# Kernel tuning notes

Hardware: AMD Instinct MI355X
Metric: run time of the kernel (lower is better)

## Reference

```python
import jax, jax.numpy as jnp
import numpy as np

B, S, H, P2 = 64, 512, 768, 46  # batch, seq, hidden, num_p*2


def setup_inputs() -> dict:
    key = jax.random.key(0)
    k1, k2, k3, k4 = jax.random.split(key, 4)
    hidden_states = jax.random.normal(k1, (B, S, H), dtype=jnp.float32)
    # subject start/end indices must lie within the valid (masked-in) prefix
    lengths = jax.random.randint(k2, (B,), S // 4, S + 1)  # cue lengths per sample
    input_mask = (jnp.arange(S)[None, :] < lengths[:, None]).astype(jnp.int32)
    ids = jax.random.randint(k3, (B, 2), 0, S // 4)
    batch_subject_ids = jnp.sort(ids, axis=1).astype(jnp.int32)
    W = jax.random.normal(k4, (P2, H), dtype=jnp.float32) * (1.0 / np.sqrt(H))
    b = jnp.zeros((P2,), dtype=jnp.float32)
    return {"hidden_states": hidden_states, "batch_subject_ids": batch_subject_ids,
            "input_mask": input_mask, "W": W, "b": b}


def reference(hidden_states, batch_subject_ids, input_mask, W, b):
    # per-sample subject embedding: h[b, start] + h[b, end]  -> [B, H]
    batch_idx = jnp.arange(hidden_states.shape[0])
    s = (hidden_states[batch_idx, batch_subject_ids[:, 0]]
         + hidden_states[batch_idx, batch_subject_ids[:, 1]])
    # broadcast-add s to the first cue_len positions of each sample
    cue_len = jnp.sum(input_mask, axis=1)  # [B]
    pos_mask = (jnp.arange(hidden_states.shape[1])[None, :] < cue_len[:, None])  # [B, S]
    h = hidden_states + s[:, None, :] * pos_mask[:, :, None].astype(hidden_states.dtype)
    # linear + sigmoid^4 (dropout is identity in eval mode)
    logits = jnp.einsum('bsh,ph->bsp', h, W) + b
    return jax.nn.sigmoid(logits) ** 4
```

## Files before the change

kernel.cpp:

```cpp
#include <hip/hip_runtime.h>

#define SEQ 512
#define HID 768
#define P2  46
#define BLK 256
#define WST 776

typedef short bf16x8 __attribute__((ext_vector_type(8)));
typedef float f32x4  __attribute__((ext_vector_type(4)));

__device__ __forceinline__ unsigned short f2bf(float f) {
  union { float f; unsigned int u; } v; v.f = f;
  return (unsigned short)((v.u + 0x7FFFu + ((v.u >> 16) & 1u)) >> 16);
}

__global__ __launch_bounds__(BLK) void fused_kernel(const float* __restrict__ h,
                                                    const int* __restrict__ ids,
                                                    const int* __restrict__ mask,
                                                    const float* __restrict__ W,
                                                    const float* __restrict__ bias,
                                                    float* __restrict__ out) {
  __shared__ __align__(16) unsigned short wlds[48 * WST];
  __shared__ __align__(16) float s_lds[HID];
  __shared__ float q_lds[48];

  const int tid  = threadIdx.x;
  const int lane = tid & 63, wv = tid >> 6;
  const int mr   = lane & 15, qd = lane >> 4;
  const int row0 = blockIdx.x * 64;
  const int b    = row0 >> 9;
  const int rowa = row0 + (wv << 4) + mr;
  const float* hrow = h + (size_t)rowa * HID + (qd << 3);

  for (int i = tid; i < WST; i += BLK)
    ((unsigned int*)(wlds + 46 * WST))[i] = 0u;
  for (int i = tid; i < (P2 * HID) / 4; i += BLK) {
    int f = i * 4;
    int r = f / HID;
    int c = f - r * HID;
    float4 w4 = *(const float4*)(W + (size_t)r * HID + c);
    ushort4 v;
    v.x = f2bf(w4.x); v.y = f2bf(w4.y); v.z = f2bf(w4.z); v.w = f2bf(w4.w);
    *(ushort4*)&wlds[r * WST + c] = v;
  }
  {
    int i0 = ids[b * 2 + 0], i1 = ids[b * 2 + 1];
    const float* r0 = h + ((size_t)b * SEQ + i0) * HID;
    const float* r1 = h + ((size_t)b * SEQ + i1) * HID;
    #pragma unroll
    for (int j = 0; j < HID / BLK; ++j) {
      int k = tid + j * BLK;
      s_lds[k] = r0[k] + r1[k];
    }
  }
  __syncthreads();

  if (tid < P2 * 4) {
    int p = tid >> 2, kq = tid & 3;
    const float4* wp = (const float4*)(W + (size_t)p * HID + kq * 192);
    float acc = 0.f;
    #pragma unroll 8
    for (int j = 0; j < 48; ++j) {
      float4 w4 = wp[j];
      int k = kq * 192 + j * 4;
      acc += s_lds[k] * w4.x + s_lds[k + 1] * w4.y
           + s_lds[k + 2] * w4.z + s_lds[k + 3] * w4.w;
    }
    acc += __shfl_xor(acc, 1, 64);
    acc += __shfl_xor(acc, 2, 64);
    if (kq == 0) q_lds[p] = acc;
  }
  __syncthreads();

  f32x4 acc[3];
  #pragma unroll
  for (int nt = 0; nt < 3; ++nt) acc[nt] = f32x4{0.f, 0.f, 0.f, 0.f};

  #pragma unroll
  for (int half = 0; half < 2; ++half) {
    const float* hb = hrow + half * 384;
    float4 abuf[24];
    #pragma unroll
    for (int i = 0; i < 24; ++i)
      abuf[i] = *(const float4*)(hb + (i >> 1) * 32 + (i & 1) * 4);
    #pragma unroll
    for (int it = 0; it < 12; ++it) {
      bf16x8 a;
      {
        float4 x0 = abuf[2 * it], x1 = abuf[2 * it + 1];
        a[0] = (short)f2bf(x0.x); a[1] = (short)f2bf(x0.y);
        a[2] = (short)f2bf(x0.z); a[3] = (short)f2bf(x0.w);
        a[4] = (short)f2bf(x1.x); a[5] = (short)f2bf(x1.y);
        a[6] = (short)f2bf(x1.z); a[7] = (short)f2bf(x1.w);
      }
      #pragma unroll
      for (int nt = 0; nt < 3; ++nt) {
        bf16x8 bb = *(const bf16x8*)&wlds[((nt << 4) + mr) * WST
                                          + half * 384 + it * 32 + (qd << 3)];
        acc[nt] = __builtin_amdgcn_mfma_f32_16x16x32_bf16(a, bb, acc[nt], 0, 0, 0);
      }
    }
  }

  int mrow[4];
  #pragma unroll
  for (int i = 0; i < 4; ++i)
    mrow[i] = mask[row0 + (wv << 4) + (qd << 2) + i];

  #pragma unroll
  for (int nt = 0; nt < 3; ++nt) {
    int p = (nt << 4) + mr;
    if (p < P2) {
      float bv = bias[p];
      float qv = q_lds[p];
      #pragma unroll
      for (int i = 0; i < 4; ++i) {
        int row = row0 + (wv << 4) + (qd << 2) + i;
        float x = acc[nt][i] + bv + (mrow[i] ? qv : 0.f);
        float sg = 1.f / (1.f + __expf(-x));
        sg *= sg; sg *= sg;
        out[(size_t)row * P2 + p] = sg;
      }
    }
  }
}

extern "C" void kernel_launch(void* const* d_in, const int* in_sizes, int n_in,
                              void* d_out, int out_size, void* d_ws, size_t ws_size,
                              hipStream_t stream) {
  const float* h    = (const float*)d_in[0];
  const int*   ids  = (const int*)d_in[1];
  const int*   mask = (const int*)d_in[2];
  const float* W    = (const float*)d_in[3];
  const float* bias = (const float*)d_in[4];
  float* out = (float*)d_out;

  fused_kernel<<<dim3((64 * SEQ) / 64), BLK, 0, stream>>>(h, ids, mask, W, bias, out);
}
```

Measured before the change: 179.7 us.

## Stream hidden-state chunks into LDS with async global_load_lds multi-buffering

Replaces the register-staged loads of each row's hidden states with a four-buffer pipeline of async global-to-LDS loads in 32-column chunks. The LDS layout is XOR-swizzled, and s_waitcnt vmcnt controls when each chunk is ready. The block grows to 512 threads covering 128 rows, so the per-block bf16 conversion of W and the subject-vector projection are amortized over twice as many rows. Each wave loads and reads only its own 16 rows, so no barrier is needed between chunks, but correctness depends on the hand-written vmcnt counts. The larger LDS footprint may limit occupancy.

```diff
diff --git a/kernel.cpp b/kernel.cpp
--- a/kernel.cpp
+++ b/kernel.cpp
@@ -3,7 +3,10 @@
 #define SEQ 512
 #define HID 768
 #define P2  46
-#define BLK 256
+#define BLK 512
+#define MT  128
+#define KC  32
+#define NC  (HID / KC)
 #define WST 776
 
 typedef short bf16x8 __attribute__((ext_vector_type(8)));
@@ -14,44 +17,59 @@
   return (unsigned short)((v.u + 0x7FFFu + ((v.u >> 16) & 1u)) >> 16);
 }
 
-__global__ __launch_bounds__(BLK) void fused_kernel(const float* __restrict__ h,
-                                                    const int* __restrict__ ids,
-                                                    const int* __restrict__ mask,
-                                                    const float* __restrict__ W,
-                                                    const float* __restrict__ bias,
-                                                    float* __restrict__ out) {
+__device__ __forceinline__ void gl_lds16(const float* g, void* l) {
+  __builtin_amdgcn_global_load_lds(
+      (const __attribute__((address_space(1))) void*)g,
+      (__attribute__((address_space(3))) void*)l, 16, 0, 0);
+}
+
+__global__ __launch_bounds__(BLK, 2) void fused_kernel(const float* __restrict__ h,
+                                                       const int* __restrict__ ids,
+                                                       const int* __restrict__ mask,
+                                                       const float* __restrict__ W,
+                                                       const float* __restrict__ bias,
+                                                       float* __restrict__ out) {
   __shared__ __align__(16) unsigned short wlds[48 * WST];
+  __shared__ __align__(16) float hbuf[4][MT * KC];
   __shared__ __align__(16) float s_lds[HID];
   __shared__ float q_lds[48];
 
   const int tid  = threadIdx.x;
   const int lane = tid & 63, wv = tid >> 6;
   const int mr   = lane & 15, qd = lane >> 4;
-  const int row0 = blockIdx.x * 64;
+  const int row0 = blockIdx.x * MT;
   const int b    = row0 >> 9;
-  const int rowa = row0 + (wv << 4) + mr;
-  const float* hrow = h + (size_t)rowa * HID + (qd << 3);
 
-  for (int i = tid; i < WST; i += BLK)
+  auto issueChunk = [&](int c) {
+    int buf = c & 3;
+    #pragma unroll
+    for (int j = 0; j < 2; ++j) {
+      int sb  = (wv << 7) + (j << 6);
+      int s   = sb + lane;
+      int row = s >> 3;
+      int cc  = (s & 7) ^ (row & 7);
+      const float* g = h + (size_t)(row0 + row) * HID + c * KC + (cc << 2);
+      gl_lds16(g, (void*)&hbuf[buf][sb << 2]);
+    }
+  };
+
+  issueChunk(0); issueChunk(1); issueChunk(2);
+
+  for (int i = tid; i < (2 * WST) / 2; i += BLK)
     ((unsigned int*)(wlds + 46 * WST))[i] = 0u;
   for (int i = tid; i < (P2 * HID) / 4; i += BLK) {
-    int f = i * 4;
-    int r = f / HID;
-    int c = f - r * HID;
-    float4 w4 = *(const float4*)(W + (size_t)r * HID + c);
+    int r  = i / 192;
+    int c0 = (i - r * 192) * 4;
+    float4 w4 = *(const float4*)(W + (size_t)r * HID + c0);
     ushort4 v;
     v.x = f2bf(w4.x); v.y = f2bf(w4.y); v.z = f2bf(w4.z); v.w = f2bf(w4.w);
-    *(ushort4*)&wlds[r * WST + c] = v;
+    *(ushort4*)&wlds[r * WST + c0] = v;
   }
   {
     int i0 = ids[b * 2 + 0], i1 = ids[b * 2 + 1];
     const float* r0 = h + ((size_t)b * SEQ + i0) * HID;
     const float* r1 = h + ((size_t)b * SEQ + i1) * HID;
-    #pragma unroll
-    for (int j = 0; j < HID / BLK; ++j) {
-      int k = tid + j * BLK;
-      s_lds[k] = r0[k] + r1[k];
-    }
+    for (int k = tid; k < HID; k += BLK) s_lds[k] = r0[k] + r1[k];
   }
   __syncthreads();
 
@@ -76,30 +94,32 @@
   #pragma unroll
   for (int nt = 0; nt < 3; ++nt) acc[nt] = f32x4{0.f, 0.f, 0.f, 0.f};
 
+  const int rA   = (wv << 4) + mr;
+  const int base = (rA & 15) * 8 + (wv << 7);
+  const int r7   = mr & 7;
+
   #pragma unroll
-  for (int half = 0; half < 2; ++half) {
-    const float* hb = hrow + half * 384;
-    float4 abuf[24];
+  for (int c = 0; c < NC; ++c) {
+    const int fut = NC - 1 - c;
+    if (fut >= 2)      asm volatile("s_waitcnt vmcnt(4)" ::: "memory");
+    else if (fut == 1) asm volatile("s_waitcnt vmcnt(2)" ::: "memory");
+    else               asm volatile("s_waitcnt vmcnt(0)" ::: "memory");
+
+    const float* hb = &hbuf[c & 3][0];
+    int cc0 = qd << 1;
+    float4 x0 = *(const float4*)&hb[(base + (cc0 ^ r7)) << 2];
+    float4 x1 = *(const float4*)&hb[(base + ((cc0 + 1) ^ r7)) << 2];
+    bf16x8 a;
+    a[0] = (short)f2bf(x0.x); a[1] = (short)f2bf(x0.y);
+    a[2] = (short)f2bf(x0.z); a[3] = (short)f2bf(x0.w);
+    a[4] = (short)f2bf(x1.x); a[5] = (short)f2bf(x1.y);
+    a[6] = (short)f2bf(x1.z); a[7] = (short)f2bf(x1.w);
     #pragma unroll
-    for (int i = 0; i < 24; ++i)
-      abuf[i] = *(const float4*)(hb + (i >> 1) * 32 + (i & 1) * 4);
-    #pragma unroll
-    for (int it = 0; it < 12; ++it) {
-      bf16x8 a;
-      {
-        float4 x0 = abuf[2 * it], x1 = abuf[2 * it + 1];
-        a[0] = (short)f2bf(x0.x); a[1] = (short)f2bf(x0.y);
-        a[2] = (short)f2bf(x0.z); a[3] = (short)f2bf(x0.w);
-        a[4] = (short)f2bf(x1.x); a[5] = (short)f2bf(x1.y);
-        a[6] = (short)f2bf(x1.z); a[7] = (short)f2bf(x1.w);
-      }
-      #pragma unroll
-      for (int nt = 0; nt < 3; ++nt) {
-        bf16x8 bb = *(const bf16x8*)&wlds[((nt << 4) + mr) * WST
-                                          + half * 384 + it * 32 + (qd << 3)];
-        acc[nt] = __builtin_amdgcn_mfma_f32_16x16x32_bf16(a, bb, acc[nt], 0, 0, 0);
-      }
+    for (int nt = 0; nt < 3; ++nt) {
+      bf16x8 bb = *(const bf16x8*)&wlds[((nt << 4) + mr) * WST + c * KC + (qd << 3)];
+      acc[nt] = __builtin_amdgcn_mfma_f32_16x16x32_bf16(a, bb, acc[nt], 0, 0, 0);
     }
+    if (c + 3 < NC) issueChunk(c + 3);
   }
 
   int mrow[4];
@@ -135,5 +155,5 @@
   const float* bias = (const float*)d_in[4];
   float* out = (float*)d_out;
 
-  fused_kernel<<<dim3((64 * SEQ) / 64), BLK, 0, stream>>>(h, ids, mask, W, bias, out);
+  fused_kernel<<<dim3((64 * SEQ) / MT), BLK, 0, stream>>>(h, ids, mask, W, bias, out);
 }
```

Result: faster. 169.5 us (-5.7%).
